# Kernel optimization log

Measured on AMD Instinct MI355X. Metric: run time of the kernel, lower is better.

## Reference

```python
import jax, jax.numpy as jnp
import numpy as np

B, T, E = 2, 2048, 2048
H, KV, D = 16, 4, 128
N_REP = H // KV
WINDOW = 512
BASE_THETA = 10000.0
MIN_VAL = -1e9


def _rope_cos_sin(seq_len, dim, dtype):
    inv_freq = 1.0 / (BASE_THETA ** (jnp.arange(0, dim, 2, dtype=jnp.float32) / dim))
    ang = jnp.arange(seq_len, dtype=jnp.float32)[:, None] * inv_freq[None, :]  # [T, D/2]
    return jnp.cos(ang).astype(dtype), jnp.sin(ang).astype(dtype)


def _apply_rope(x, cos, sin):
    # x: [B, T, h, D]; rotate-half convention
    x1, x2 = jnp.split(x, 2, axis=-1)
    c = cos[None, :, None, :]
    s = sin[None, :, None, :]
    return jnp.concatenate([x1 * c - x2 * s, x2 * c + x1 * s], axis=-1)


def setup_inputs() -> dict:
    key = jax.random.key(0)
    k1, k2, k3, k4, k5 = jax.random.split(key, 5)
    std = 0.02 / np.sqrt(2 * 24)
    return {
        "x": jax.random.normal(k1, (B, T, E), dtype=jnp.float32),
        "Wq": jax.random.normal(k2, (H * D, E), dtype=jnp.float32) * std,
        "Wk": jax.random.normal(k3, (KV * D, E), dtype=jnp.float32) * std,
        "Wv": jax.random.normal(k4, (KV * D, E), dtype=jnp.float32) * std,
        "Wo": jax.random.normal(k5, (E, E), dtype=jnp.float32) * std,
    }


def reference(x, Wq, Wk, Wv, Wo):
    b, t, e = x.shape
    scale = 1.0 / jnp.sqrt(jnp.float32(D))

    q = (x @ Wq.T).reshape(b, t, H, D)
    k = (x @ Wk.T).reshape(b, t, KV, D)
    v = (x @ Wv.T).reshape(b, t, KV, D)

    cos, sin = _rope_cos_sin(t, D, x.dtype)
    q = _apply_rope(q, cos, sin)
    k = _apply_rope(k, cos, sin)

    # GQA: repeat kv heads to match query heads
    k = jnp.repeat(k, N_REP, axis=2)  # [B, T, H, D]
    v = jnp.repeat(v, N_REP, axis=2)

    scores = jnp.einsum("bqhd,bkhd->bhqk", q, k) * scale  # [B, H, T, T]

    # sliding-window causal additive mask (offset=0)
    rows = jnp.arange(t)[:, None]
    cols = jnp.arange(t)[None, :]
    valid = (cols <= rows) & ((rows - cols) < WINDOW)
    mask = jnp.where(valid, 0.0, MIN_VAL).astype(x.dtype)  # [T, T]
    scores = scores + mask[None, None, :, :]

    attn = jax.nn.softmax(scores, axis=-1)
    out = jnp.einsum("bhqk,bkhd->bqhd", attn, v).reshape(b, t, H * D)
    return out @ Wo.T
```

## Files before the change

kernel.cpp:

```cpp
#include <hip/hip_runtime.h>
#include <hip/hip_bf16.h>
#include <cstdint>

#define TSEQ 2048
#define NB   2
#define NH   16
#define NKV  4
#define HD   128
#define EMB  2048
#define WIN  512

typedef unsigned short u16;
typedef __attribute__((ext_vector_type(8))) short s16x8;
typedef __attribute__((ext_vector_type(4))) float f32x4;
typedef __attribute__((ext_vector_type(16))) float f32x16;
typedef __attribute__((ext_vector_type(4))) unsigned short u16x4;
typedef __attribute__((ext_vector_type(8))) unsigned short u16x8;

__device__ __forceinline__ u16 f2bf(float x) {
    unsigned u = __builtin_bit_cast(unsigned, x);
    u += 0x7fffu + ((u >> 16) & 1u);
    return (u16)(u >> 16);
}
__device__ __forceinline__ float bf2f(u16 u) {
    return __builtin_bit_cast(float, ((unsigned)u) << 16);
}
__device__ __forceinline__ float ex2(float x) {
    return __builtin_amdgcn_exp2f(x);
}

__device__ __forceinline__ void gld_lds16(const void* g, void* l) {
    __builtin_amdgcn_global_load_lds(
        (__attribute__((address_space(1))) void*)(void*)(g),
        (__attribute__((address_space(3))) void*)(l),
        16, 0, 0);
}

__device__ __forceinline__ f32x4 mfma16(s16x8 a, s16x8 b, f32x4 c) {
    return __builtin_amdgcn_mfma_f32_16x16x32_bf16(a, b, c, 0, 0, 0);
}
__device__ __forceinline__ f32x16 mfma32(s16x8 a, s16x8 b, f32x16 c) {
    return __builtin_amdgcn_mfma_f32_32x32x16_bf16(a, b, c, 0, 0, 0);
}

template <int CTRL>
__device__ __forceinline__ float dpp_movf(float x) {
    return __builtin_bit_cast(float,
        __builtin_amdgcn_update_dpp(0, __builtin_bit_cast(int, x), CTRL, 0xF, 0xF, true));
}
__device__ __forceinline__ float dpp_max16(float x) {
    x = fmaxf(x, dpp_movf<0xB1>(x));
    x = fmaxf(x, dpp_movf<0x4E>(x));
    x = fmaxf(x, dpp_movf<0x128>(x));
    x = fmaxf(x, dpp_movf<0x124>(x));
    return x;
}
__device__ __forceinline__ float dpp_sum16(float x) {
    x += dpp_movf<0xB1>(x);
    x += dpp_movf<0x4E>(x);
    x += dpp_movf<0x128>(x);
    x += dpp_movf<0x124>(x);
    return x;
}

__global__ void cast_all(const float* __restrict__ x,  const float* __restrict__ wq,
                         const float* __restrict__ wk, const float* __restrict__ wv,
                         const float* __restrict__ wo,
                         u16* __restrict__ xb, u16* __restrict__ wqb,
                         u16* __restrict__ wkvb, u16* __restrict__ wob,
                         float* __restrict__ tab) {
    if (blockIdx.x >= 18432) {
        int i = (blockIdx.x - 18432) * 256 + threadIdx.x;
        int t = i >> 6, d = i & 63;
        float inv = __expf(-(float)d * (9.210340371976184f / 64.0f));
        float s, c;
        sincosf((float)t * inv, &s, &c);
        tab[i] = c;
        tab[131072 + i] = s;
        return;
    }
    long i = ((long)blockIdx.x * 256 + threadIdx.x) * 4;
    const float* s; u16* d; long off;
    if (i < 8388608L)        { s = x;  d = xb;             off = i; }
    else if (i < 12582912L)  { s = wq; d = wqb;            off = i - 8388608L; }
    else if (i < 13631488L)  { s = wk; d = wkvb;           off = i - 12582912L; }
    else if (i < 14680064L)  { s = wv; d = wkvb + 1048576; off = i - 13631488L; }
    else                     { s = wo; d = wob;            off = i - 14680064L; }
    float4 v = *(const float4*)(s + off);
    u16x4 o;
    o[0] = f2bf(v.x); o[1] = f2bf(v.y); o[2] = f2bf(v.z); o[3] = f2bf(v.w);
    *(u16x4*)(d + off) = o;
}

template <int MODE>
__global__ __launch_bounds__(256) void gemm_bt(const u16* __restrict__ A, const u16* __restrict__ B,
                                               void* __restrict__ Cp, u16* __restrict__ vtp,
                                               u16* __restrict__ kp,
                                               int M, int N, int K) {
    __shared__ __align__(16) u16 smem[16384];
    u16* As = smem;
    u16* Bs = smem + 8192;
    const int tid  = threadIdx.x;
    const int lane = tid & 63;
    const int w    = tid >> 6;
    const int l31  = lane & 31;
    const int half = lane >> 5;
    const int wr   = w >> 1, wc = w & 1;

    const int srow   = w * 8 + (lane >> 3);
    const int schunk = lane & 7;
    const u16* agp[4];
    const u16* bgp[4];
#pragma unroll
    for (int s = 0; s < 4; s++) {
        const int row = s * 32 + srow;
        const int sig = ((row >> 1) ^ (row >> 2)) & 7;
        agp[s] = A + (size_t)(blockIdx.y * 128 + row) * K + (schunk ^ sig) * 8;
        bgp[s] = B + (size_t)(blockIdx.x * 128 + row) * K + (schunk ^ sig) * 8;
    }

    int sigA[2], sigB[2];
#pragma unroll
    for (int i = 0; i < 2; i++) {
        const int ra = wr * 64 + i * 32 + l31;
        sigA[i] = ((ra >> 1) ^ (ra >> 2)) & 7;
        const int rb = wc * 64 + i * 32 + l31;
        sigB[i] = ((rb >> 1) ^ (rb >> 2)) & 7;
    }

    f32x16 acc[2][2];
#pragma unroll
    for (int i = 0; i < 2; i++)
#pragma unroll
        for (int j = 0; j < 2; j++)
#pragma unroll
            for (int r = 0; r < 16; r++)
                acc[i][j][r] = 0.f;

    for (int k0 = 0; k0 < K; k0 += 64) {
#pragma unroll
        for (int s = 0; s < 4; s++) {
            gld_lds16(agp[s], (char*)As + (s * 32 + w * 8) * 128);
            agp[s] += 64;
        }
#pragma unroll
        for (int s = 0; s < 4; s++) {
            gld_lds16(bgp[s], (char*)Bs + (s * 32 + w * 8) * 128);
            bgp[s] += 64;
        }
        __syncthreads();
        s16x8 af[2][4], bf[2][4];
#pragma unroll
        for (int i = 0; i < 2; i++)
#pragma unroll
            for (int ks = 0; ks < 4; ks++)
                af[i][ks] = *(const s16x8*)((char*)As + (wr * 64 + i * 32 + l31) * 128 +
                                            ((half + ks * 2) ^ sigA[i]) * 16);
#pragma unroll
        for (int j = 0; j < 2; j++)
#pragma unroll
            for (int ks = 0; ks < 4; ks++)
                bf[j][ks] = *(const s16x8*)((char*)Bs + (wc * 64 + j * 32 + l31) * 128 +
                                            ((half + ks * 2) ^ sigB[j]) * 16);
#pragma unroll
        for (int ks = 0; ks < 4; ks++)
#pragma unroll
            for (int i = 0; i < 2; i++)
#pragma unroll
                for (int j = 0; j < 2; j++)
                    acc[i][j] = mfma32(af[i][ks], bf[j][ks], acc[i][j]);
        __syncthreads();
    }

    const int row0 = blockIdx.y * 128 + wr * 64;
    const int col0 = blockIdx.x * 128 + wc * 64 + l31;

    if (MODE == 0) {
#pragma unroll
        for (int i = 0; i < 2; i++)
#pragma unroll
            for (int j = 0; j < 2; j++)
#pragma unroll
                for (int r = 0; r < 16; r++) {
                    const int crow = row0 + i * 32 + (r & 3) + 8 * (r >> 2) + 4 * half;
                    ((float*)Cp)[(size_t)crow * N + col0 + j * 32] = acc[i][j][r];
                }
    } else {
        if (blockIdx.x < 16) {
#pragma unroll
            for (int i = 0; i < 2; i++)
#pragma unroll
                for (int j = 0; j < 2; j++)
#pragma unroll
                    for (int r = 0; r < 16; r++) {
                        const int crow = row0 + i * 32 + (r & 3) + 8 * (r >> 2) + 4 * half;
                        ((u16*)Cp)[(size_t)crow * 2048 + col0 + j * 32] = f2bf(acc[i][j][r]);
                    }
        } else if (blockIdx.x < 20) {
            const int kcol0 = col0 - 2048;
#pragma unroll
            for (int i = 0; i < 2; i++)
#pragma unroll
                for (int j = 0; j < 2; j++)
#pragma unroll
                    for (int r = 0; r < 16; r++) {
                        const int crow = row0 + i * 32 + (r & 3) + 8 * (r >> 2) + 4 * half;
                        kp[(size_t)crow * 512 + kcol0 + j * 32] = f2bf(acc[i][j][r]);
                    }
        } else {
            const int kvi = blockIdx.x - 20;
            const int bb  = (blockIdx.y * 128) >> 11;
            const int tl0 = (blockIdx.y * 128) & (TSEQ - 1);
            u16* tr = smem;
#pragma unroll
            for (int p = 0; p < 2; p++) {
                __syncthreads();
                if (wc == p) {
#pragma unroll
                    for (int i = 0; i < 2; i++)
#pragma unroll
                        for (int j = 0; j < 2; j++)
#pragma unroll
                            for (int r = 0; r < 16; r++) {
                                const int tl = wr * 64 + i * 32 + (r & 3) + 8 * (r >> 2) + 4 * half;
                                tr[(j * 32 + l31) * 136 + tl] = f2bf(acc[i][j][r]);
                            }
                }
                __syncthreads();
#pragma unroll
                for (int s = 0; s < 4; s++) {
                    int slot = s * 256 + tid;
                    int dr = slot >> 4;
                    int tc = slot & 15;
                    u16x8 val = *(const u16x8*)(tr + dr * 136 + tc * 8);
                    *(u16x8*)(vtp + ((size_t)((bb * NKV + kvi) * HD + p * 64 + dr)) * TSEQ +
                              tl0 + tc * 8) = val;
                }
            }
        }
    }
}

__global__ void rope_k(u16* __restrict__ buf, const float* __restrict__ tab) {
    int i = blockIdx.x * 256 + threadIdx.x;
    int d   = i & 63;
    int hh  = (i >> 6) & 3;
    int row = i >> 8;
    int t   = row & (TSEQ - 1);
    size_t base = (size_t)row * 512 + hh * HD + d;
    float x1 = bf2f(buf[base]);
    float x2 = bf2f(buf[base + 64]);
    float c = tab[t * 64 + d];
    float s = tab[131072 + t * 64 + d];
    buf[base]      = f2bf(x1 * c - x2 * s);
    buf[base + 64] = f2bf(x2 * c + x1 * s);
}

__global__ __launch_bounds__(256, 3) void attn_kernel(const u16* __restrict__ qb, const u16* __restrict__ kb,
                                                      const u16* __restrict__ vt, const float* __restrict__ tab,
                                                      u16* __restrict__ ao) {
    __shared__ __align__(16) char smem[40960];
    u16* ks = (u16*)smem;
    u16* vs = (u16*)(smem + 16384);
    u16* Pl = (u16*)(smem + 32768);

    const int tid  = threadIdx.x;
    const int w    = tid >> 6;
    const int lane = tid & 63;
    const int l15  = lane & 15;
    const int quad = lane >> 4;
    const int id   = blockIdx.x;
    const int kv   = id & 3;
    const int b    = (id >> 2) & 1;
    const int q0   = (id >> 3) * 16;
    const int h    = kv * 4 + w;
    u16* Pw = Pl + w * 1024;
    const float scale2 = 0.1275174089593282f;

    const u16* kbase = kb + (size_t)b * TSEQ * 512 + kv * HD;
    const u16* vbase = vt + (size_t)(b * NKV + kv) * HD * TSEQ;

    s16x8 aq[4];
    {
        const u16* qrow = qb + (size_t)(b * TSEQ + q0 + l15) * EMB + h * HD + quad * 8;
        const float* ct = tab + (size_t)(q0 + l15) * 64 + quad * 8;
        float qf[4][8], cs[2][8], sn[2][8];
        *(float4*)(&cs[0][0]) = *(const float4*)(ct);
        *(float4*)(&cs[0][4]) = *(const float4*)(ct + 4);
        *(float4*)(&cs[1][0]) = *(const float4*)(ct + 32);
        *(float4*)(&cs[1][4]) = *(const float4*)(ct + 36);
        *(float4*)(&sn[0][0]) = *(const float4*)(ct + 131072);
        *(float4*)(&sn[0][4]) = *(const float4*)(ct + 131076);
        *(float4*)(&sn[1][0]) = *(const float4*)(ct + 131104);
        *(float4*)(&sn[1][4]) = *(const float4*)(ct + 131108);
#pragma unroll
        for (int c = 0; c < 4; c++)
#pragma unroll
            for (int e = 0; e < 8; e++)
                qf[c][e] = bf2f(qrow[c * 32 + e]);
#pragma unroll
        for (int c = 0; c < 2; c++)
#pragma unroll
            for (int e = 0; e < 8; e++) {
                float x1 = qf[c][e], x2 = qf[c + 2][e];
                qf[c][e]     = x1 * cs[c][e] - x2 * sn[c][e];
                qf[c + 2][e] = x2 * cs[c][e] + x1 * sn[c][e];
            }
#pragma unroll
        for (int c = 0; c < 4; c++)
#pragma unroll
            for (int e = 0; e < 8; e++)
                aq[c][e] = (short)f2bf(qf[c][e]);
    }

    f32x4 o[8];
#pragma unroll
    for (int n = 0; n < 8; n++) o[n] = f32x4{0.f, 0.f, 0.f, 0.f};
    float mrow[4] = {-1e30f, -1e30f, -1e30f, -1e30f};
    float lrow[4] = {0.f, 0.f, 0.f, 0.f};

    int kb0 = q0 - (WIN - 1);
    if (kb0 < 0) kb0 = 0;
    kb0 &= ~63;

    for (int kbi = kb0; kbi <= q0 + 15; kbi += 64) {
#pragma unroll
        for (int s = 0; s < 4; s++) {
            int slot = s * 256 + tid;
            int i    = slot >> 4;
            int lc   = (slot & 15) ^ (i & 7);
            gld_lds16(kbase + (size_t)(kbi + i) * 512 + lc * 8, (char*)ks + slot * 16);
        }
#pragma unroll
        for (int s = 0; s < 4; s++) {
            int slot = s * 256 + tid;
            int d    = slot >> 3;
            int lc   = (slot & 7) ^ (d & 7);
            gld_lds16(vbase + (size_t)d * TSEQ + kbi + lc * 8, (char*)vs + slot * 16);
        }
        __syncthreads();

        f32x4 sv[4];
#pragma unroll
        for (int kt = 0; kt < 4; kt++) sv[kt] = f32x4{0.f, 0.f, 0.f, 0.f};
#pragma unroll
        for (int c = 0; c < 4; c++) {
            s16x8 bk[4];
#pragma unroll
            for (int kt = 0; kt < 4; kt++) {
                int sc = (c * 4 + quad) ^ (l15 & 7);
                bk[kt] = *(const s16x8*)(ks + (kt * 16 + l15) * 128 + sc * 8);
            }
#pragma unroll
            for (int kt = 0; kt < 4; kt++)
                sv[kt] = mfma16(aq[c], bk[kt], sv[kt]);
        }

        const bool full = (kbi >= q0 - 496) && (kbi + 63 <= q0);
        float alpha[4], p[4][4];
#pragma unroll
        for (int r = 0; r < 4; r++) {
            const int row = q0 + quad * 4 + r;
            float v[4];
            if (full) {
#pragma unroll
                for (int kt = 0; kt < 4; kt++) v[kt] = sv[kt][r] * scale2;
            } else {
#pragma unroll
                for (int kt = 0; kt < 4; kt++) {
                    int cidx = kbi + kt * 16 + l15;
                    v[kt] = (cidx <= row && row - cidx < WIN) ? sv[kt][r] * scale2 : -1e30f;
                }
            }
            float mx = fmaxf(fmaxf(v[0], v[1]), fmaxf(v[2], v[3]));
            mx = dpp_max16(mx);
            float mnew = fmaxf(mrow[r], mx);
            alpha[r] = ex2(mrow[r] - mnew);
            float e0 = ex2(v[0] - mnew);
            float e1 = ex2(v[1] - mnew);
            float e2 = ex2(v[2] - mnew);
            float e3 = ex2(v[3] - mnew);
            float rs = (e0 + e1) + (e2 + e3);
            rs = dpp_sum16(rs);
            lrow[r] = lrow[r] * alpha[r] + rs;
            mrow[r] = mnew;
            p[0][r] = e0; p[1][r] = e1; p[2][r] = e2; p[3][r] = e3;
        }
#pragma unroll
        for (int n = 0; n < 8; n++) {
            o[n][0] *= alpha[0]; o[n][1] *= alpha[1];
            o[n][2] *= alpha[2]; o[n][3] *= alpha[3];
        }

#pragma unroll
        for (int r = 0; r < 4; r++)
#pragma unroll
            for (int kt = 0; kt < 4; kt++)
                Pw[(kt >> 1) * 512 + (quad * 4 + r) * 32 + (kt & 1) * 16 + l15] = f2bf(p[kt][r]);
        asm volatile("s_waitcnt lgkmcnt(0)" ::: "memory");
        s16x8 ap0 = *(const s16x8*)(Pw + l15 * 32 + quad * 8);
        s16x8 ap1 = *(const s16x8*)(Pw + 512 + l15 * 32 + quad * 8);

#pragma unroll
        for (int n = 0; n < 8; n++) {
            int sc = quad ^ (l15 & 7);
            s16x8 bv = *(const s16x8*)(vs + (n * 16 + l15) * 64 + sc * 8);
            o[n] = mfma16(ap0, bv, o[n]);
        }
#pragma unroll
        for (int n = 0; n < 8; n++) {
            int sc = (4 + quad) ^ (l15 & 7);
            s16x8 bv = *(const s16x8*)(vs + (n * 16 + l15) * 64 + sc * 8);
            o[n] = mfma16(ap1, bv, o[n]);
        }
        __syncthreads();
    }

    float linv[4];
#pragma unroll
    for (int r = 0; r < 4; r++) linv[r] = 1.0f / lrow[r];
    u16* Ow = (u16*)(smem + w * 4352);
#pragma unroll
    for (int n = 0; n < 8; n++)
#pragma unroll
        for (int r = 0; r < 4; r++)
            Ow[(quad * 4 + r) * 136 + n * 16 + l15] = f2bf(o[n][r] * linv[r]);
    asm volatile("s_waitcnt lgkmcnt(0)" ::: "memory");
#pragma unroll
    for (int s = 0; s < 4; s++) {
        int row = s * 4 + quad;
        u16x8 val = *(const u16x8*)(Ow + row * 136 + l15 * 8);
        *(u16x8*)(ao + (size_t)(b * TSEQ + q0 + row) * EMB + h * HD + l15 * 8) = val;
    }
}

extern "C" void kernel_launch(void* const* d_in, const int* in_sizes, int n_in,
                              void* d_out, int out_size, void* d_ws, size_t ws_size,
                              hipStream_t stream) {
    const float* x  = (const float*)d_in[0];
    const float* Wq = (const float*)d_in[1];
    const float* Wk = (const float*)d_in[2];
    const float* Wv = (const float*)d_in[3];
    const float* Wo = (const float*)d_in[4];
    float* out = (float*)d_out;

    u16* ws   = (u16*)d_ws;
    u16* xb   = ws;
    u16* wqb  = ws + 8388608L;
    u16* wkvb = ws + 12582912L;
    u16* wob  = ws + 14680064L;
    u16* qb   = ws + 18874368L;
    u16* kbuf = ws + 27262976L;
    u16* vt   = ws + 29360128L;
    float* tab = (float*)(ws + 31457280L);
    u16* ao   = xb;

    cast_all<<<18944, 256, 0, stream>>>(x, Wq, Wk, Wv, Wo, xb, wqb, wkvb, wob, tab);

    gemm_bt<3><<<dim3(24, 32), 256, 0, stream>>>(xb, wqb, qb, vt, kbuf, 4096, 3072, 2048);

    rope_k<<<4096, 256, 0, stream>>>(kbuf, tab);

    attn_kernel<<<1024, 256, 0, stream>>>(qb, kbuf, vt, tab, ao);

    gemm_bt<0><<<dim3(16, 32), 256, 0, stream>>>(ao, wob, out, nullptr, nullptr, 4096, 2048, 2048);
}
```

Measured before the change: 267.8 us.

## Fuse K RoPE into QKV GEMM, double-buffer K in attention, retile O-proj

Applies RoPE to K inside the QKV GEMM epilogue through an LDS-staged tile, removing the separate rope_k kernel launch and its read-modify-write pass. In attention, K tiles are double-buffered in LDS with prefetch of the next block, and V fragments are loaded straight from global memory into registers instead of through LDS. This drops one barrier per iteration. The output projection moves to its own kernel with 64x128 tiles, doubling the grid to improve CU occupancy. Risks: more register pressure in attention, and uncoalesced, LDS-bypassing V loads.

```diff
diff --git a/kernel.cpp b/kernel.cpp
--- a/kernel.cpp
+++ b/kernel.cpp
@@ -92,11 +92,10 @@
     *(u16x4*)(d + off) = o;
 }
 
-template <int MODE>
-__global__ __launch_bounds__(256) void gemm_bt(const u16* __restrict__ A, const u16* __restrict__ B,
-                                               void* __restrict__ Cp, u16* __restrict__ vtp,
-                                               u16* __restrict__ kp,
-                                               int M, int N, int K) {
+__global__ __launch_bounds__(256) void gemm_qkv(const u16* __restrict__ A, const u16* __restrict__ B,
+                                                u16* __restrict__ qp, u16* __restrict__ vtp,
+                                                u16* __restrict__ kp, const float* __restrict__ tab,
+                                                int M, int N, int K) {
     __shared__ __align__(16) u16 smem[16384];
     u16* As = smem;
     u16* Bs = smem + 8192;
@@ -175,7 +174,7 @@
     const int row0 = blockIdx.y * 128 + wr * 64;
     const int col0 = blockIdx.x * 128 + wc * 64 + l31;
 
-    if (MODE == 0) {
+    if (blockIdx.x < 16) {
 #pragma unroll
         for (int i = 0; i < 2; i++)
 #pragma unroll
@@ -183,85 +182,174 @@
 #pragma unroll
                 for (int r = 0; r < 16; r++) {
                     const int crow = row0 + i * 32 + (r & 3) + 8 * (r >> 2) + 4 * half;
-                    ((float*)Cp)[(size_t)crow * N + col0 + j * 32] = acc[i][j][r];
+                    qp[(size_t)crow * 2048 + col0 + j * 32] = f2bf(acc[i][j][r]);
                 }
+    } else if (blockIdx.x < 20) {
+        const int kvi = blockIdx.x - 16;
+        u16* tr = smem;
+#pragma unroll
+        for (int p = 0; p < 2; p++) {
+            __syncthreads();
+            if (wr == p) {
+#pragma unroll
+                for (int i = 0; i < 2; i++)
+#pragma unroll
+                    for (int j = 0; j < 2; j++)
+#pragma unroll
+                        for (int r = 0; r < 16; r++) {
+                            const int tl = i * 32 + (r & 3) + 8 * (r >> 2) + 4 * half;
+                            tr[tl * 128 + wc * 64 + j * 32 + l31] = f2bf(acc[i][j][r]);
+                        }
+            }
+            __syncthreads();
+#pragma unroll
+            for (int s = 0; s < 4; s++) {
+                int slot = s * 256 + tid;
+                int dr = slot >> 4;
+                int dc = slot & 15;
+                int grow = blockIdx.y * 128 + p * 64 + dr;
+                int t = grow & (TSEQ - 1);
+                u16x8 a  = *(const u16x8*)(tr + dr * 128 + dc * 8);
+                u16x8 bp = *(const u16x8*)(tr + dr * 128 + (dc ^ 8) * 8);
+                const float* ct = tab + (size_t)t * 64 + (dc & 7) * 8;
+                float sgn = (dc < 8) ? -1.f : 1.f;
+                u16x8 outv;
+#pragma unroll
+                for (int e = 0; e < 8; e++) {
+                    float cc = ct[e];
+                    float ss = ct[131072 + e];
+                    outv[e] = f2bf(bf2f(a[e]) * cc + sgn * bf2f(bp[e]) * ss);
+                }
+                *(u16x8*)(kp + (size_t)grow * 512 + kvi * 128 + dc * 8) = outv;
+            }
+        }
     } else {
-        if (blockIdx.x < 16) {
-#pragma unroll
-            for (int i = 0; i < 2; i++)
-#pragma unroll
-                for (int j = 0; j < 2; j++)
-#pragma unroll
-                    for (int r = 0; r < 16; r++) {
-                        const int crow = row0 + i * 32 + (r & 3) + 8 * (r >> 2) + 4 * half;
-                        ((u16*)Cp)[(size_t)crow * 2048 + col0 + j * 32] = f2bf(acc[i][j][r]);
-                    }
-        } else if (blockIdx.x < 20) {
-            const int kcol0 = col0 - 2048;
-#pragma unroll
-            for (int i = 0; i < 2; i++)
-#pragma unroll
-                for (int j = 0; j < 2; j++)
-#pragma unroll
-                    for (int r = 0; r < 16; r++) {
-                        const int crow = row0 + i * 32 + (r & 3) + 8 * (r >> 2) + 4 * half;
-                        kp[(size_t)crow * 512 + kcol0 + j * 32] = f2bf(acc[i][j][r]);
-                    }
-        } else {
-            const int kvi = blockIdx.x - 20;
-            const int bb  = (blockIdx.y * 128) >> 11;
-            const int tl0 = (blockIdx.y * 128) & (TSEQ - 1);
-            u16* tr = smem;
-#pragma unroll
-            for (int p = 0; p < 2; p++) {
-                __syncthreads();
-                if (wc == p) {
-#pragma unroll
-                    for (int i = 0; i < 2; i++)
-#pragma unroll
-                        for (int j = 0; j < 2; j++)
-#pragma unroll
-                            for (int r = 0; r < 16; r++) {
-                                const int tl = wr * 64 + i * 32 + (r & 3) + 8 * (r >> 2) + 4 * half;
-                                tr[(j * 32 + l31) * 136 + tl] = f2bf(acc[i][j][r]);
-                            }
-                }
-                __syncthreads();
-#pragma unroll
-                for (int s = 0; s < 4; s++) {
-                    int slot = s * 256 + tid;
-                    int dr = slot >> 4;
-                    int tc = slot & 15;
-                    u16x8 val = *(const u16x8*)(tr + dr * 136 + tc * 8);
-                    *(u16x8*)(vtp + ((size_t)((bb * NKV + kvi) * HD + p * 64 + dr)) * TSEQ +
-                              tl0 + tc * 8) = val;
-                }
-            }
-        }
-    }
-}
-
-__global__ void rope_k(u16* __restrict__ buf, const float* __restrict__ tab) {
-    int i = blockIdx.x * 256 + threadIdx.x;
-    int d   = i & 63;
-    int hh  = (i >> 6) & 3;
-    int row = i >> 8;
-    int t   = row & (TSEQ - 1);
-    size_t base = (size_t)row * 512 + hh * HD + d;
-    float x1 = bf2f(buf[base]);
-    float x2 = bf2f(buf[base + 64]);
-    float c = tab[t * 64 + d];
-    float s = tab[131072 + t * 64 + d];
-    buf[base]      = f2bf(x1 * c - x2 * s);
-    buf[base + 64] = f2bf(x2 * c + x1 * s);
+        const int kvi = blockIdx.x - 20;
+        const int bb  = (blockIdx.y * 128) >> 11;
+        const int tl0 = (blockIdx.y * 128) & (TSEQ - 1);
+        u16* tr = smem;
+#pragma unroll
+        for (int p = 0; p < 2; p++) {
+            __syncthreads();
+            if (wc == p) {
+#pragma unroll
+                for (int i = 0; i < 2; i++)
+#pragma unroll
+                    for (int j = 0; j < 2; j++)
+#pragma unroll
+                        for (int r = 0; r < 16; r++) {
+                            const int tl = wr * 64 + i * 32 + (r & 3) + 8 * (r >> 2) + 4 * half;
+                            tr[(j * 32 + l31) * 136 + tl] = f2bf(acc[i][j][r]);
+                        }
+            }
+            __syncthreads();
+#pragma unroll
+            for (int s = 0; s < 4; s++) {
+                int slot = s * 256 + tid;
+                int dr = slot >> 4;
+                int tc = slot & 15;
+                u16x8 val = *(const u16x8*)(tr + dr * 136 + tc * 8);
+                *(u16x8*)(vtp + ((size_t)((bb * NKV + kvi) * HD + p * 64 + dr)) * TSEQ +
+                          tl0 + tc * 8) = val;
+            }
+        }
+    }
+}
+
+__global__ __launch_bounds__(256) void gemm_o(const u16* __restrict__ A, const u16* __restrict__ B,
+                                              float* __restrict__ C, int M, int N, int K) {
+    __shared__ __align__(16) u16 smem[12288];
+    u16* As = smem;
+    u16* Bs = smem + 4096;
+    const int tid  = threadIdx.x;
+    const int lane = tid & 63;
+    const int w    = tid >> 6;
+    const int l31  = lane & 31;
+    const int half = lane >> 5;
+    const int wr   = w >> 1, wc = w & 1;
+
+    const int srow   = w * 8 + (lane >> 3);
+    const int schunk = lane & 7;
+    const u16* agp[2];
+    const u16* bgp[4];
+#pragma unroll
+    for (int s = 0; s < 2; s++) {
+        const int row = s * 32 + srow;
+        const int sig = ((row >> 1) ^ (row >> 2)) & 7;
+        agp[s] = A + (size_t)(blockIdx.y * 64 + row) * K + (schunk ^ sig) * 8;
+    }
+#pragma unroll
+    for (int s = 0; s < 4; s++) {
+        const int row = s * 32 + srow;
+        const int sig = ((row >> 1) ^ (row >> 2)) & 7;
+        bgp[s] = B + (size_t)(blockIdx.x * 128 + row) * K + (schunk ^ sig) * 8;
+    }
+
+    int sigA;
+    {
+        const int ra = wr * 32 + l31;
+        sigA = ((ra >> 1) ^ (ra >> 2)) & 7;
+    }
+    int sigB[2];
+#pragma unroll
+    for (int j = 0; j < 2; j++) {
+        const int rb = wc * 64 + j * 32 + l31;
+        sigB[j] = ((rb >> 1) ^ (rb >> 2)) & 7;
+    }
+
+    f32x16 acc[2];
+#pragma unroll
+    for (int j = 0; j < 2; j++)
+#pragma unroll
+        for (int r = 0; r < 16; r++)
+            acc[j][r] = 0.f;
+
+    for (int k0 = 0; k0 < K; k0 += 64) {
+#pragma unroll
+        for (int s = 0; s < 2; s++) {
+            gld_lds16(agp[s], (char*)As + (s * 32 + w * 8) * 128);
+            agp[s] += 64;
+        }
+#pragma unroll
+        for (int s = 0; s < 4; s++) {
+            gld_lds16(bgp[s], (char*)Bs + (s * 32 + w * 8) * 128);
+            bgp[s] += 64;
+        }
+        __syncthreads();
+        s16x8 af[4], bf[2][4];
+#pragma unroll
+        for (int ks = 0; ks < 4; ks++)
+            af[ks] = *(const s16x8*)((char*)As + (wr * 32 + l31) * 128 +
+                                     ((half + ks * 2) ^ sigA) * 16);
+#pragma unroll
+        for (int j = 0; j < 2; j++)
+#pragma unroll
+            for (int ks = 0; ks < 4; ks++)
+                bf[j][ks] = *(const s16x8*)((char*)Bs + (wc * 64 + j * 32 + l31) * 128 +
+                                            ((half + ks * 2) ^ sigB[j]) * 16);
+#pragma unroll
+        for (int ks = 0; ks < 4; ks++)
+#pragma unroll
+            for (int j = 0; j < 2; j++)
+                acc[j] = mfma32(af[ks], bf[j][ks], acc[j]);
+        __syncthreads();
+    }
+
+    const int row0 = blockIdx.y * 64 + wr * 32;
+    const int col0 = blockIdx.x * 128 + wc * 64 + l31;
+#pragma unroll
+    for (int j = 0; j < 2; j++)
+#pragma unroll
+        for (int r = 0; r < 16; r++) {
+            const int crow = row0 + (r & 3) + 8 * (r >> 2) + 4 * half;
+            C[(size_t)crow * N + col0 + j * 32] = acc[j][r];
+        }
 }
 
 __global__ __launch_bounds__(256, 3) void attn_kernel(const u16* __restrict__ qb, const u16* __restrict__ kb,
                                                       const u16* __restrict__ vt, const float* __restrict__ tab,
                                                       u16* __restrict__ ao) {
     __shared__ __align__(16) char smem[40960];
-    u16* ks = (u16*)smem;
-    u16* vs = (u16*)(smem + 16384);
     u16* Pl = (u16*)(smem + 32768);
 
     const int tid  = threadIdx.x;
@@ -279,6 +367,16 @@
 
     const u16* kbase = kb + (size_t)b * TSEQ * 512 + kv * HD;
     const u16* vbase = vt + (size_t)(b * NKV + kv) * HD * TSEQ;
+
+    auto stageK = [&](int krow0, char* dst) {
+#pragma unroll
+        for (int s = 0; s < 4; s++) {
+            int slot = s * 256 + tid;
+            int i    = slot >> 4;
+            int lc   = (slot & 15) ^ (i & 7);
+            gld_lds16(kbase + (size_t)(krow0 + i) * 512 + lc * 8, dst + slot * 16);
+        }
+    };
 
     s16x8 aq[4];
     {
@@ -323,23 +421,19 @@
     if (kb0 < 0) kb0 = 0;
     kb0 &= ~63;
 
+    stageK(kb0, smem);
+    int pp = 0;
+
     for (int kbi = kb0; kbi <= q0 + 15; kbi += 64) {
-#pragma unroll
-        for (int s = 0; s < 4; s++) {
-            int slot = s * 256 + tid;
-            int i    = slot >> 4;
-            int lc   = (slot & 15) ^ (i & 7);
-            gld_lds16(kbase + (size_t)(kbi + i) * 512 + lc * 8, (char*)ks + slot * 16);
-        }
-#pragma unroll
-        for (int s = 0; s < 4; s++) {
-            int slot = s * 256 + tid;
-            int d    = slot >> 3;
-            int lc   = (slot & 7) ^ (d & 7);
-            gld_lds16(vbase + (size_t)d * TSEQ + kbi + lc * 8, (char*)vs + slot * 16);
-        }
         __syncthreads();
 
+        const u16* vb = vbase + (size_t)l15 * TSEQ + kbi + quad * 8;
+        s16x8 vf0[8];
+#pragma unroll
+        for (int n = 0; n < 8; n++)
+            vf0[n] = *(const s16x8*)(vb + (size_t)n * 16 * TSEQ);
+
+        u16* ks = (u16*)(smem + pp * 16384);
         f32x4 sv[4];
 #pragma unroll
         for (int kt = 0; kt < 4; kt++) sv[kt] = f32x4{0.f, 0.f, 0.f, 0.f};
@@ -386,6 +480,15 @@
             mrow[r] = mnew;
             p[0][r] = e0; p[1][r] = e1; p[2][r] = e2; p[3][r] = e3;
         }
+
+        s16x8 vf1[8];
+#pragma unroll
+        for (int n = 0; n < 8; n++)
+            vf1[n] = *(const s16x8*)(vb + 32 + (size_t)n * 16 * TSEQ);
+
+        if (kbi + 64 <= q0 + 15)
+            stageK(kbi + 64, smem + (pp ^ 1) * 16384);
+
 #pragma unroll
         for (int n = 0; n < 8; n++) {
             o[n][0] *= alpha[0]; o[n][1] *= alpha[1];
@@ -402,19 +505,15 @@
         s16x8 ap1 = *(const s16x8*)(Pw + 512 + l15 * 32 + quad * 8);
 
 #pragma unroll
-        for (int n = 0; n < 8; n++) {
-            int sc = quad ^ (l15 & 7);
-            s16x8 bv = *(const s16x8*)(vs + (n * 16 + l15) * 64 + sc * 8);
-            o[n] = mfma16(ap0, bv, o[n]);
-        }
-#pragma unroll
-        for (int n = 0; n < 8; n++) {
-            int sc = (4 + quad) ^ (l15 & 7);
-            s16x8 bv = *(const s16x8*)(vs + (n * 16 + l15) * 64 + sc * 8);
-            o[n] = mfma16(ap1, bv, o[n]);
-        }
-        __syncthreads();
-    }
+        for (int n = 0; n < 8; n++)
+            o[n] = mfma16(ap0, vf0[n], o[n]);
+#pragma unroll
+        for (int n = 0; n < 8; n++)
+            o[n] = mfma16(ap1, vf1[n], o[n]);
+
+        pp ^= 1;
+    }
+    __syncthreads();
 
     float linv[4];
 #pragma unroll
@@ -457,11 +556,9 @@
 
     cast_all<<<18944, 256, 0, stream>>>(x, Wq, Wk, Wv, Wo, xb, wqb, wkvb, wob, tab);
 
-    gemm_bt<3><<<dim3(24, 32), 256, 0, stream>>>(xb, wqb, qb, vt, kbuf, 4096, 3072, 2048);
-
-    rope_k<<<4096, 256, 0, stream>>>(kbuf, tab);
+    gemm_qkv<<<dim3(24, 32), 256, 0, stream>>>(xb, wqb, qb, vt, kbuf, tab, 4096, 3072, 2048);
 
     attn_kernel<<<1024, 256, 0, stream>>>(qb, kbuf, vt, tab, ao);
 
-    gemm_bt<0><<<dim3(16, 32), 256, 0, stream>>>(ao, wob, out, nullptr, nullptr, 4096, 2048, 2048);
-}
+    gemm_o<<<dim3(16, 64), 256, 0, stream>>>(ao, wob, out, 4096, 2048, 2048);
+}
```

Measured after the change: 334.9 us. 25.0% more time.
